# Kernel optimization log

Measured on AMD Instinct MI355X. Metric: run time of the kernel, lower is better.

## Reference

```python
import jax, jax.numpy as jnp
import numpy as np

N, E, ESM, H, OUT, L, NG = 20000, 640000, 1280, 128, 256, 3, 64
NV, EV = 4, 1  # node/edge vector channels
MSG_S, MSG_V = 2 * H + H, 2 * NV + EV   # 384, 9
UPD_S, UPD_V = 2 * H, 2 * NV            # 256, 8


def _safe_norm(v):
    # exact ||v|| with zero (not nan) gradient at v == 0
    n2 = jnp.sum(v * v, axis=-1)
    pos = n2 > 0
    return jnp.sqrt(jnp.where(pos, n2, 1.0)) * pos


def _normalize(x, eps=1e-12):
    n = _safe_norm(x)[..., None]
    return jnp.where(n > 0, x / jnp.maximum(n, eps), 0.0)


def _ln(x, g, b, eps=1e-5):
    m = x.mean(-1, keepdims=True)
    v = ((x - m) ** 2).mean(-1, keepdims=True)
    return (x - m) / jnp.sqrt(v + eps) * g + b


def _gvp(s, v, Wss, Wvs, Wsv, Wvv, g, b):
    # s: [M, Cs], v: [M, Cv, 3]
    vn = _safe_norm(v)                                        # [M, Cv]
    s_out = jax.nn.gelu(_ln(s @ Wss.T + vn @ Wvs.T, g, b), approximate=False)
    v_out = jnp.einsum('mic,oi->moc', v, Wvv)                 # [M, Cvo, 3]
    v_out = v_out * jax.nn.sigmoid(s @ Wsv.T)[:, :, None]     # gate from input s
    return s_out, v_out


def _compute_node_vectors(coords, cb):
    ca_cb = _normalize(cb - coords)
    ca_next = jnp.roll(coords, -1, axis=0)
    d = (ca_next - coords).at[-1].set(0.0)
    d = _normalize(d)
    normal = _normalize(jnp.cross(ca_cb, d))
    t = (ca_next - jnp.roll(coords, 1, axis=0)).at[0].set(0.0).at[-1].set(0.0)
    t = _normalize(t)
    return jnp.stack([ca_cb, d, normal, t], axis=1)           # [N, 4, 3]


def setup_inputs() -> dict:
    key = jax.random.key(0)
    ks = jax.random.split(key, 32)

    def w(k, shape):
        return (jax.random.normal(k, shape, jnp.float32) / np.sqrt(shape[-1])).astype(jnp.float32)

    inp = {
        'esm_features': jax.random.normal(ks[0], (N, ESM), jnp.float32),
        'geometric_features': jax.random.normal(ks[1], (N, 15), jnp.float32),
        'node_coords': jax.random.normal(ks[2], (N, 3), jnp.float32) * 10.0,
        'edge_index': jax.random.randint(ks[3], (2, E), 0, N, jnp.int32),
        'edge_attr': jax.random.normal(ks[4], (E, 16), jnp.float32),
        'batch_index': jnp.sort(jax.random.randint(ks[5], (N,), 0, NG, jnp.int32)),
        # projections
        'node_proj_W': w(ks[6], (H, ESM + 9)), 'node_proj_b': jnp.zeros((H,), jnp.float32),
        'edge_proj_W': w(ks[7], (H, 13)), 'edge_proj_b': jnp.zeros((H,), jnp.float32),
        # message GVP (stacked over L layers)
        'msg_Wss': w(ks[8], (L, H, MSG_S)), 'msg_Wvs': w(ks[9], (L, H, MSG_V)),
        'msg_Wsv': w(ks[10], (L, NV, MSG_S)), 'msg_Wvv': w(ks[11], (L, NV, MSG_V)),
        'msg_ln_g': jnp.ones((L, H), jnp.float32), 'msg_ln_b': jnp.zeros((L, H), jnp.float32),
        # update GVP
        'upd_Wss': w(ks[12], (L, H, UPD_S)), 'upd_Wvs': w(ks[13], (L, H, UPD_V)),
        'upd_Wsv': w(ks[14], (L, NV, UPD_S)), 'upd_Wvv': w(ks[15], (L, NV, UPD_V)),
        'upd_ln_g': jnp.ones((L, H), jnp.float32), 'upd_ln_b': jnp.zeros((L, H), jnp.float32),
        # heads
        'node_out_W': w(ks[16], (ESM, H)), 'node_out_b': jnp.zeros((ESM,), jnp.float32),
        'graph_out_W': w(ks[17], (OUT, H)), 'graph_out_b': jnp.zeros((OUT,), jnp.float32),
    }
    return inp


def reference(esm_features, geometric_features, node_coords, edge_index, edge_attr,
              batch_index, node_proj_W, node_proj_b, edge_proj_W, edge_proj_b,
              msg_Wss, msg_Wvs, msg_Wsv, msg_Wvv, msg_ln_g, msg_ln_b,
              upd_Wss, upd_Wvs, upd_Wsv, upd_Wvv, upd_ln_g, upd_ln_b,
              node_out_W, node_out_b, graph_out_W, graph_out_b):
    n = esm_features.shape[0]
    cb = geometric_features[:, 3:6]
    geo_scalar = geometric_features[:, 6:15]
    node_s = jnp.concatenate([esm_features, geo_scalar], -1) @ node_proj_W.T + node_proj_b
    node_v = _compute_node_vectors(node_coords, cb)
    edge_s = jnp.concatenate([edge_attr[:, 0:2], edge_attr[:, 5:]], -1) @ edge_proj_W.T + edge_proj_b
    edge_v = edge_attr[:, 2:5][:, None, :]                    # [E, 1, 3]
    src, dst = edge_index[0], edge_index[1]
    for l in range(msg_Wss.shape[0]):
        ms = jnp.concatenate([node_s[src], node_s[dst], edge_s], -1)   # [E, 3H]
        mv = jnp.concatenate([node_v[src], node_v[dst], edge_v], 1)    # [E, 9, 3]
        ms, mv = _gvp(ms, mv, msg_Wss[l], msg_Wvs[l], msg_Wsv[l], msg_Wvv[l],
                      msg_ln_g[l], msg_ln_b[l])
        ag_s = jnp.zeros((n, ms.shape[1]), ms.dtype).at[dst].add(ms)
        ag_v = jnp.zeros((n, mv.shape[1], 3), mv.dtype).at[dst].add(mv)
        us = jnp.concatenate([node_s, ag_s], -1)
        uv = jnp.concatenate([node_v, ag_v], 1)
        ns, nv = _gvp(us, uv, upd_Wss[l], upd_Wvs[l], upd_Wsv[l], upd_Wvv[l],
                      upd_ln_g[l], upd_ln_b[l])
        node_s = node_s + ns
        node_v = node_v + nv
    updated_nodes = node_s @ node_out_W.T + node_out_b
    gfeat = node_s @ graph_out_W.T + graph_out_b
    cnt = jax.ops.segment_sum(jnp.ones((n,), gfeat.dtype), batch_index, NG)
    graph_emb = jax.ops.segment_sum(gfeat, batch_index, NG) / jnp.maximum(cnt, 1.0)[:, None]
    return graph_emb, updated_nodes
```

## Files before the change

kernel.cpp:

```cpp
#include <hip/hip_runtime.h>
#include <math.h>

#define DEVI __device__ __forceinline__

namespace {

constexpr int NN = 20000;
constexpr int NE = 640000;

DEVI float gelu_f(float x){ return 0.5f*x*(1.0f+erff(x*0.70710678118654752440f)); }
DEVI float gelu_t(float x){
  float u = x*x;
  float z = x*(1.59576912f + 0.07135481f*u);
  return x / (1.f + __expf(-z));
}
DEVI float sigm(float x){ return 1.0f/(1.0f+expf(-x)); }
DEVI float sigm_f(float x){ return 1.0f/(1.0f+__expf(-x)); }
DEVI unsigned bf_rne(float f){ unsigned u=__float_as_uint(f); return (u + 0x7fffu + ((u>>16)&1u)) >> 16; }

struct F3{ float x,y,z; };
DEVI F3 sub3(F3 a, F3 b){ return F3{a.x-b.x, a.y-b.y, a.z-b.z}; }
DEVI F3 cross3(F3 a, F3 b){ return F3{a.y*b.z-a.z*b.y, a.z*b.x-a.x*b.z, a.x*b.y-a.y*b.x}; }
DEVI F3 snorm3(F3 v){
  float n2 = v.x*v.x+v.y*v.y+v.z*v.z;
  if(n2 > 0.f){ float inv = 1.0f/sqrtf(n2); return F3{v.x*inv, v.y*inv, v.z*inv}; }
  return F3{0.f,0.f,0.f};
}

__global__ void k_prep(const float* __restrict__ npW, const float* __restrict__ noW,
                       const float* __restrict__ goW,
                       const float* __restrict__ mWss, const float* __restrict__ mWvs,
                       const float* __restrict__ uWss, const float* __restrict__ uWvs,
                       float* __restrict__ Wt_np, float* __restrict__ Wt_no,
                       float* __restrict__ Wt_go,
                       float* __restrict__ Wt_mss, float* __restrict__ Wt_mvs,
                       float* __restrict__ Wt_uss, float* __restrict__ Wt_uvs){
  int b = blockIdx.x, t = threadIdx.x;
  const float* src; float* dst; int R,C,ld,base,elems;
  if(b<645){ src=npW; dst=Wt_np; R=128;C=1289;ld=1289; base=0; elems=164992; }
  else if(b<1285){ src=noW; dst=Wt_no; R=1280;C=128;ld=128; base=645; elems=163840; }
  else if(b<1413){ src=goW; dst=Wt_go; R=256;C=128;ld=128; base=1285; elems=32768; }
  else {
    int bb=b-1413; int l=bb/265; int r=bb-l*265;
    if(r<128){ src=mWss+(size_t)l*128*384; dst=Wt_mss+(size_t)l*256*128; R=128;C=256;ld=384; base=1413+l*265; elems=32768; }
    else if(r<133){ src=mWvs+(size_t)l*128*9; dst=Wt_mvs+(size_t)l*9*128; R=128;C=9;ld=9; base=1413+l*265+128; elems=1152; }
    else if(r<261){ src=uWss+(size_t)l*128*256; dst=Wt_uss+(size_t)l*256*128; R=128;C=256;ld=256; base=1413+l*265+133; elems=32768; }
    else { src=uWvs+(size_t)l*128*8; dst=Wt_uvs+(size_t)l*8*128; R=128;C=8;ld=8; base=1413+l*265+261; elems=1024; }
  }
  int idx=(b-base)*256+t;
  if(idx>=elems) return;
  int r=idx/C, c=idx%C;
  dst[c*R+r] = src[r*ld+c];
}

__global__ __launch_bounds__(256,4) void k_init(
                       const float* __restrict__ esm, const float* __restrict__ geo,
                       const float* __restrict__ Wt, const float* __restrict__ bias,
                       float* __restrict__ node_s){
  __shared__ float s_l[16][64];
  int t = threadIdx.x;
  int o = t&127, h = t>>7;
  int n0 = blockIdx.x*16;
  float acc[8];
#pragma unroll
  for(int i=0;i<8;i++) acc[i]=0.f;
  for(int k0=0;k0<1289;k0+=64){
    int kmax = (1289-k0 < 64) ? (1289-k0) : 64;
    for(int idx=t; idx<1024; idx+=256){
      int n = idx>>6, k = idx&63;
      float v = 0.f;
      int kk = k0+k;
      if(k < kmax){
        v = (kk<1280) ? esm[(size_t)(n0+n)*1280 + kk] : geo[(n0+n)*15 + 6 + (kk-1280)];
      }
      s_l[n][k] = v;
    }
    __syncthreads();
    int kq = kmax & ~3;
    for(int k=0;k<kq;k+=4){
      float w0 = Wt[(k0+k)*128+o];
      float w1 = Wt[(k0+k+1)*128+o];
      float w2 = Wt[(k0+k+2)*128+o];
      float w3 = Wt[(k0+k+3)*128+o];
#pragma unroll
      for(int n=0;n<8;n++){
        float4 s4 = *reinterpret_cast<const float4*>(&s_l[h*8+n][k]);
        acc[n] += s4.x*w0 + s4.y*w1 + s4.z*w2 + s4.w*w3;
      }
    }
    for(int k=kq;k<kmax;k++){
      float w = Wt[(k0+k)*128+o];
#pragma unroll
      for(int n=0;n<8;n++) acc[n] += s_l[h*8+n][k]*w;
    }
    __syncthreads();
  }
  float b = bias[o];
#pragma unroll
  for(int n=0;n<8;n++) node_s[(size_t)(n0+h*8+n)*128 + o] = acc[n] + b;
}

__global__ void k_nodevec(const float* __restrict__ coords, const float* __restrict__ geo,
                          float* __restrict__ node_v,
                          int* __restrict__ counts, int* __restrict__ cntg){
  int n = blockIdx.x*256 + threadIdx.x;
  if(n<64) cntg[n]=0;
  if(n>=NN) return;
  counts[n]=0;
  F3 c  {coords[n*3], coords[n*3+1], coords[n*3+2]};
  F3 cb {geo[n*15+3], geo[n*15+4], geo[n*15+5]};
  F3 cacb = snorm3(sub3(cb, c));
  F3 d{0.f,0.f,0.f};
  if(n < NN-1){
    F3 nx {coords[(n+1)*3], coords[(n+1)*3+1], coords[(n+1)*3+2]};
    d = snorm3(sub3(nx, c));
  }
  F3 nor = snorm3(cross3(cacb, d));
  F3 tv{0.f,0.f,0.f};
  if(n>0 && n<NN-1){
    F3 nx {coords[(n+1)*3], coords[(n+1)*3+1], coords[(n+1)*3+2]};
    F3 pv {coords[(n-1)*3], coords[(n-1)*3+1], coords[(n-1)*3+2]};
    tv = snorm3(sub3(nx, pv));
  }
  float* p = node_v + n*12;
  p[0]=cacb.x; p[1]=cacb.y; p[2]=cacb.z;
  p[3]=d.x;    p[4]=d.y;    p[5]=d.z;
  p[6]=nor.x;  p[7]=nor.y;  p[8]=nor.z;
  p[9]=tv.x;   p[10]=tv.y;  p[11]=tv.z;
}

__global__ void k_hist(const int* __restrict__ eidx, const int* __restrict__ batch,
                       int* __restrict__ counts, int* __restrict__ cntg){
  int i = blockIdx.x*256+threadIdx.x;
  if(i<NE) atomicAdd(&counts[eidx[NE+i]], 1);
  if(i<NN) atomicAdd(&cntg[batch[i]], 1);
}
__global__ void k_scan1(const int* __restrict__ counts, int* __restrict__ bsums){
  __shared__ int red[256];
  int b=blockIdx.x, t=threadIdx.x;
  int base=b*512;
  int v=0;
  for(int i=t;i<512;i+=256){ int g=base+i; if(g<NN) v+=counts[g]; }
  red[t]=v; __syncthreads();
  for(int s=128;s;s>>=1){ if(t<s) red[t]+=red[t+s]; __syncthreads(); }
  if(t==0) bsums[b]=red[0];
}
__global__ void k_scan23(const int* __restrict__ counts, const int* __restrict__ bsums,
                         int* __restrict__ offs, int* __restrict__ cursor){
  __shared__ int c_l[512];
  int b=blockIdx.x, t=threadIdx.x, base=b*512;
  for(int i=t;i<512;i+=256){ int g=base+i; c_l[i] = (g<NN)? counts[g]:0; }
  __syncthreads();
  if(t==0){
    int run=0;
    for(int i=0;i<b;i++) run += bsums[i];
    for(int i=0;i<512;i++){
      int g=base+i;
      if(g<NN){ offs[g]=run; cursor[g]=run; }
      run += c_l[i];
    }
    if(b==39) offs[NN]=run;
  }
}
__global__ void k_fill(const int* __restrict__ eidx, int* __restrict__ cursor,
                       const float* __restrict__ eattr,
                       int* __restrict__ srcp, float* __restrict__ ea_s){
  int e = blockIdx.x*256+threadIdx.x;
  if(e>=NE) return;
  int d = eidx[NE+e];
  int s = eidx[e];
  int pos = atomicAdd(&cursor[d], 1);
  srcp[pos] = s;
  const float4* src4 = reinterpret_cast<const float4*>(eattr + (size_t)e*16);
  float4* dst4 = reinterpret_cast<float4*>(ea_s + (size_t)pos*16);
  dst4[0]=src4[0]; dst4[1]=src4[1]; dst4[2]=src4[2]; dst4[3]=src4[3];
}

__global__ __launch_bounds__(256,4) void k_pre(
                      const float* __restrict__ node_s, const float* __restrict__ node_v,
                      const float* __restrict__ Wt_ss, const float* __restrict__ Wt_vs,
                      const float* __restrict__ Wsv, const float* __restrict__ Wvv,
                      float* __restrict__ P_a, float* __restrict__ P_b,
                      float* __restrict__ G_a, float* __restrict__ G_b,
                      float* __restrict__ V_a, float* __restrict__ V_b){
  __shared__ float s_l[16][128];
  __shared__ float nv_l[16][4];
  __shared__ float uv[16][12];
  int t = threadIdx.x;
  int n0 = blockIdx.x*16;
  for(int idx=t; idx<2048; idx+=256){
    int n = idx>>7, k = idx&127;
    s_l[n][k] = node_s[(size_t)(n0+n)*128 + k];
  }
  if(t<192){ int n=t/12, k=t%12; uv[n][k] = node_v[(n0+n)*12+k]; }
  __syncthreads();
  if(t<64){
    int n=t>>2, j=t&3;
    float x=uv[n][j*3], y=uv[n][j*3+1], z=uv[n][j*3+2];
    float n2=x*x+y*y+z*z;
    nv_l[n][j] = n2>0.f ? sqrtf(n2) : 0.f;
  }
  if(t<192){
    int n=t/12, k=t%12, c=k/3, x=k-c*3;
    float va=0.f, vb=0.f;
#pragma unroll
    for(int j=0;j<4;j++){
      float vv = uv[n][j*3+x];
      va += Wvv[c*9+j]*vv;
      vb += Wvv[c*9+4+j]*vv;
    }
    V_a[(n0+n)*12+k]=va; V_b[(n0+n)*12+k]=vb;
  }
  if(t<128){
    int n=t>>3, c=(t>>1)&3, hh=t&1;
    const float* w = Wsv + c*384 + hh*128;
    float g=0.f;
    for(int k=0;k<128;k+=4){
      float4 s4 = *reinterpret_cast<const float4*>(&s_l[n][k]);
      g = fmaf(s4.x,w[k],g); g = fmaf(s4.y,w[k+1],g);
      g = fmaf(s4.z,w[k+2],g); g = fmaf(s4.w,w[k+3],g);
    }
    (hh ? G_b : G_a)[(n0+n)*4+c] = g;
  }
  __syncthreads();
  int o = t&127, h = t>>7;
  float acc[16];
#pragma unroll
  for(int i=0;i<16;i++) acc[i]=0.f;
  const float* Wb = Wt_ss + h*128*128;
  for(int k=0;k<128;k+=4){
    float w0=Wb[(k+0)*128+o], w1=Wb[(k+1)*128+o], w2=Wb[(k+2)*128+o], w3=Wb[(k+3)*128+o];
#pragma unroll
    for(int n=0;n<16;n++){
      float4 s4 = *reinterpret_cast<const float4*>(&s_l[n][k]);
      acc[n] = fmaf(s4.x,w0,acc[n]); acc[n] = fmaf(s4.y,w1,acc[n]);
      acc[n] = fmaf(s4.z,w2,acc[n]); acc[n] = fmaf(s4.w,w3,acc[n]);
    }
  }
  const float* Wv = Wt_vs + h*4*128;
#pragma unroll
  for(int j=0;j<4;j++){
    float w = Wv[j*128+o];
#pragma unroll
    for(int n=0;n<16;n++) acc[n] += nv_l[n][j]*w;
  }
  float* P = h ? P_b : P_a;
#pragma unroll
  for(int n=0;n<16;n++) P[(size_t)(n0+n)*128+o] = acc[n];
}

__global__ void k_econst3(const float* __restrict__ mWss, const float* __restrict__ mWvs,
                          const float* __restrict__ mWsv, const float* __restrict__ mWvv,
                          const float* __restrict__ Wep, const float* __restrict__ epb,
                          float* __restrict__ econ){
  int l = blockIdx.x;
  const float* Wss = mWss + (size_t)l*128*384;
  const float* Wvs = mWvs + (size_t)l*128*9;
  const float* Wsv = mWsv + (size_t)l*4*384;
  const float* Wvv = mWvv + (size_t)l*4*9;
  float* ec = econ + (size_t)l*2048;
  int t=threadIdx.x;
  for(int idx=t; idx<13*128; idx+=256){
    int j=idx>>7, o=idx&127;
    float s=0.f;
    for(int k=0;k<128;k++) s += Wss[o*384+256+k]*Wep[k*13+j];
    ec[j*128+o]=s;
  }
  for(int o=t;o<128;o+=256){
    float s=0.f;
    for(int k=0;k<128;k++) s += Wss[o*384+256+k]*epb[k];
    ec[1664+o]=s;
    ec[1792+o]=Wvs[o*9+8];
  }
  if(t<52){ int c=t/13,j=t%13; float s=0.f; for(int k=0;k<128;k++) s+=Wsv[c*384+256+k]*Wep[k*13+j]; ec[1920+t]=s; }
  if(t<4){ float s=0.f; for(int k=0;k<128;k++) s+=Wsv[t*384+256+k]*epb[k]; ec[1972+t]=s; ec[1976+t]=Wvv[t*9+8]; }
}

__global__ __launch_bounds__(256,4) void k_edge(
    const float* __restrict__ ea_s, const float* __restrict__ ec,
    unsigned* __restrict__ preS2, float* __restrict__ preG){
  int t = threadIdx.x;
  int lane = t&63;
  int wid = blockIdx.x*4 + (t>>6);
  float mex[13], mey[13];
#pragma unroll
  for(int j=0;j<13;j++){ mex[j]=ec[j*128+lane]; mey[j]=ec[j*128+64+lane]; }
  float bx=ec[1664+lane], by=ec[1664+64+lane];
  float w8x=ec[1792+lane], w8y=ec[1792+64+lane];
  int cg = (lane<4)?lane:0;
  float grc[13];
#pragma unroll
  for(int j=0;j<13;j++) grc[j]=ec[1920+cg*13+j];
  float gb = ec[1972+cg];
  int e00 = wid*8;
#pragma unroll 2
  for(int i=0;i<8;i++){
    int e = e00+i;
    const float4* ea = reinterpret_cast<const float4*>(ea_s + (size_t)e*16);
    float4 A0=ea[0], A1=ea[1], A2=ea[2], A3=ea[3];
    float e0=A0.x,e1=A0.y,e2=A1.y,e3=A1.z,e4=A1.w,
          e5=A2.x,e6=A2.y,e7=A2.z,e8=A2.w,e9=A3.x,
          e10=A3.y,e11=A3.z,e12=A3.w;
    float evx=A0.z, evy=A0.w, evz=A1.x;
    float en2 = evx*evx+evy*evy+evz*evz;
    float evn = en2>0.f ? sqrtf(en2) : 0.f;
    float px = fmaf(evn,w8x,bx);
    float py = fmaf(evn,w8y,by);
    px=fmaf(mex[0],e0,px);   py=fmaf(mey[0],e0,py);
    px=fmaf(mex[1],e1,px);   py=fmaf(mey[1],e1,py);
    px=fmaf(mex[2],e2,px);   py=fmaf(mey[2],e2,py);
    px=fmaf(mex[3],e3,px);   py=fmaf(mey[3],e3,py);
    px=fmaf(mex[4],e4,px);   py=fmaf(mey[4],e4,py);
    px=fmaf(mex[5],e5,px);   py=fmaf(mey[5],e5,py);
    px=fmaf(mex[6],e6,px);   py=fmaf(mey[6],e6,py);
    px=fmaf(mex[7],e7,px);   py=fmaf(mey[7],e7,py);
    px=fmaf(mex[8],e8,px);   py=fmaf(mey[8],e8,py);
    px=fmaf(mex[9],e9,px);   py=fmaf(mey[9],e9,py);
    px=fmaf(mex[10],e10,px); py=fmaf(mey[10],e10,py);
    px=fmaf(mex[11],e11,px); py=fmaf(mey[11],e11,py);
    px=fmaf(mex[12],e12,px); py=fmaf(mey[12],e12,py);
    preS2[(size_t)e*64+lane] = bf_rne(px) | (bf_rne(py)<<16);
    if(lane<4){
      float g=gb;
      g=fmaf(grc[0],e0,g);  g=fmaf(grc[1],e1,g);  g=fmaf(grc[2],e2,g);
      g=fmaf(grc[3],e3,g);  g=fmaf(grc[4],e4,g);  g=fmaf(grc[5],e5,g);
      g=fmaf(grc[6],e6,g);  g=fmaf(grc[7],e7,g);  g=fmaf(grc[8],e8,g);
      g=fmaf(grc[9],e9,g);  g=fmaf(grc[10],e10,g); g=fmaf(grc[11],e11,g);
      g=fmaf(grc[12],e12,g);
      preG[(size_t)e*8+lane] = g;
    } else if(lane<7){
      float evv = (lane==4)?evx:((lane==5)?evy:evz);
      preG[(size_t)e*8+lane] = evv;
    }
  }
}

#define DECLST(P) unsigned P##w=0; float P##pax=0.f,P##pay=0.f,P##g8=0.f,P##ev=0.f,P##ga=0.f,P##va=0.f;
#define LOADST(P, IDX) do{ int _p=(IDX); int _s=srcp[_p]; \
  P##w   = preS2[(size_t)_p*64 + lane]; \
  P##pax = P_a[(size_t)_s*128+lane]; P##pay = P_a[(size_t)_s*128+64+lane]; \
  if(lane<12){ P##g8 = preG[(size_t)_p*8+cv]; P##ev = preG[(size_t)_p*8+4+xv]; \
               P##ga = G_a[(size_t)_s*4+cv];  P##va = V_a[(size_t)_s*12+lane]; } \
}while(0)
#define COMPUTE(P) do{ \
  float px = __uint_as_float(P##w<<16); \
  float py = __uint_as_float(P##w & 0xffff0000u); \
  float pre0 = px + P##pax + PBx; \
  float pre1 = py + P##pay + PBy; \
  float sm = pre0+pre1; \
  float sq = pre0*pre0 + pre1*pre1; \
  _Pragma("unroll") \
  for(int m=32;m;m>>=1){ sm += __shfl_xor(sm,m); sq += __shfl_xor(sq,m); } \
  float mean = sm*0.0078125f; \
  float var  = fmaf(sq,0.0078125f, -mean*mean); \
  float rstd = rsqrtf((var>0.f?var:0.f) + 1e-5f); \
  accx += gelu_t(fmaf((pre0-mean)*rstd, LGx, LBx)); \
  accy += gelu_t(fmaf((pre1-mean)*rstd, LGy, LBy)); \
  if(lane<12){ \
    float g = P##g8 + P##ga + gbn; \
    float gt = sigm_f(g); \
    avk = fmaf(fmaf(wvc, P##ev, P##va + vbk), gt, avk); \
  } \
}while(0)

__global__ __launch_bounds__(256,4) void k_msg(
                      const float* __restrict__ P_a, const float* __restrict__ P_b,
                      const float* __restrict__ G_a, const float* __restrict__ G_b,
                      const float* __restrict__ V_a, const float* __restrict__ V_b,
                      const unsigned* __restrict__ preS2, const float* __restrict__ preG,
                      const int* __restrict__ srcp, const int* __restrict__ offs,
                      const float* __restrict__ ec,
                      const float* __restrict__ lng, const float* __restrict__ lnb,
                      float* __restrict__ ag_s, float* __restrict__ ag_v){
  int t = threadIdx.x;
  int n = blockIdx.x*4 + (t>>6);
  int lane = t&63;
  float PBx = P_b[(size_t)n*128+lane], PBy = P_b[(size_t)n*128+64+lane];
  float LGx = lng[lane], LGy = lng[64+lane];
  float LBx = lnb[lane], LBy = lnb[64+lane];
  int cv = lane/3, xv = lane - cv*3;
  float vbk=0.f, gbn=0.f, wvc=0.f;
  if(lane<12){
    vbk = V_b[(size_t)n*12+lane];
    gbn = G_b[(size_t)n*4+cv];
    wvc = ec[1976+cv];
  }
  float accx=0.f, accy=0.f, avk=0.f;
  int beg = offs[n], end = offs[n+1];
  DECLST(a_) DECLST(b_)
  int idx = beg;
  if(beg < end) LOADST(a_, beg);
  while(idx + 1 < end){
    LOADST(b_, idx+1);
    COMPUTE(a_);
    if(idx + 2 < end) LOADST(a_, idx+2);
    COMPUTE(b_);
    idx += 2;
  }
  if(idx < end) COMPUTE(a_);
  ag_s[(size_t)n*128+lane]    = accx;
  ag_s[(size_t)n*128+64+lane] = accy;
  if(lane<12) ag_v[(size_t)n*12+lane] = avk;
}

__global__ __launch_bounds__(256,4) void k_update(
                         float* __restrict__ node_s, float* __restrict__ node_v,
                         const float* __restrict__ ag_s, const float* __restrict__ ag_v,
                         const float* __restrict__ Wt_ss, const float* __restrict__ Wt_vs,
                         const float* __restrict__ Wsv, const float* __restrict__ Wvv,
                         const float* __restrict__ lng, const float* __restrict__ lnb){
  __shared__ float us[16][260];
  __shared__ float pre[16][129];
  __shared__ float uv[16][24];
  __shared__ float uvn[16][8];
  __shared__ float stats[16][2];
  __shared__ float gate_l[16][4];
  int t = threadIdx.x;
  int n0 = blockIdx.x*16;
  for(int idx=t; idx<2048; idx+=256){
    int n = idx>>7, k = idx&127;
    us[n][k]     = node_s[(size_t)(n0+n)*128+k];
    us[n][128+k] = ag_s[(size_t)(n0+n)*128+k];
  }
  for(int idx=t; idx<384; idx+=256){
    int n = idx/24, k = idx%24;
    uv[n][k] = (k<12) ? node_v[(n0+n)*12+k] : ag_v[(n0+n)*12 + (k-12)];
  }
  __syncthreads();
  if(t<128){
    int n=t>>3, j=t&7;
    float x=uv[n][j*3], y=uv[n][j*3+1], z=uv[n][j*3+2];
    float n2=x*x+y*y+z*z;
    uvn[n][j] = n2>0.f ? sqrtf(n2) : 0.f;
  }
  __syncthreads();
  int o = t&127, h = t>>7;
  float acc[8];
#pragma unroll
  for(int i=0;i<8;i++) acc[i]=0.f;
  for(int k=0;k<256;k+=4){
    float w0=Wt_ss[(k+0)*128+o], w1=Wt_ss[(k+1)*128+o], w2=Wt_ss[(k+2)*128+o], w3=Wt_ss[(k+3)*128+o];
#pragma unroll
    for(int i=0;i<8;i++){
      float4 s4 = *reinterpret_cast<const float4*>(&us[h*8+i][k]);
      acc[i] = fmaf(s4.x,w0,acc[i]); acc[i] = fmaf(s4.y,w1,acc[i]);
      acc[i] = fmaf(s4.z,w2,acc[i]); acc[i] = fmaf(s4.w,w3,acc[i]);
    }
  }
#pragma unroll
  for(int j=0;j<8;j++){
    float w = Wt_vs[j*128+o];
#pragma unroll
    for(int i=0;i<8;i++) acc[i] += uvn[h*8+i][j]*w;
  }
#pragma unroll
  for(int i=0;i<8;i++) pre[h*8+i][o] = acc[i];
  __syncthreads();
  {
    int n = t>>4, p = t&15;
    float s=0.f;
#pragma unroll
    for(int q=0;q<8;q++) s += pre[n][p*8+q];
#pragma unroll
    for(int m=8;m;m>>=1) s += __shfl_xor(s,m);
    float mean = s*(1.f/128.f);
    float v=0.f;
#pragma unroll
    for(int q=0;q<8;q++){ float d=pre[n][p*8+q]-mean; v += d*d; }
#pragma unroll
    for(int m=8;m;m>>=1) v += __shfl_xor(v,m);
    if(p==0){ stats[n][0]=mean; stats[n][1]=rsqrtf(v*(1.f/128.f)+1e-5f); }
  }
  __syncthreads();
  {
    float LG = lng[o], LB = lnb[o];
#pragma unroll
    for(int i=0;i<8;i++){
      int n = h*8+i;
      float hh = (pre[n][o]-stats[n][0])*stats[n][1]*LG + LB;
      node_s[(size_t)(n0+n)*128+o] += gelu_f(hh);
    }
  }
  {
    int n = t>>4, c = t&3, p = (t>>2)&3;
    float g=0.f;
    int kb = p*64;
    for(int k=0;k<64;k+=4){
      float4 s4 = *reinterpret_cast<const float4*>(&us[n][kb+k]);
      g = fmaf(s4.x,Wsv[c*256+kb+k],g);   g = fmaf(s4.y,Wsv[c*256+kb+k+1],g);
      g = fmaf(s4.z,Wsv[c*256+kb+k+2],g); g = fmaf(s4.w,Wsv[c*256+kb+k+3],g);
    }
    g += __shfl_xor(g,4);
    g += __shfl_xor(g,8);
    if(p==0) gate_l[n][c] = sigm(g);
  }
  __syncthreads();
  if(t<192){
    int n = t/12, k = t%12, c = k/3, x = k-c*3;
    float s=0.f;
#pragma unroll
    for(int j=0;j<8;j++) s += Wvv[c*8+j]*uv[n][j*3+x];
    node_v[(n0+n)*12+k] += s*gate_l[n][c];
  }
}

__global__ __launch_bounds__(256,4) void k_outg(
                      const float* __restrict__ node_s, const float* __restrict__ Wt_no,
                      const float* __restrict__ nob, const float* __restrict__ Wt_go,
                      const int* __restrict__ batch, float* __restrict__ gacc,
                      float* __restrict__ out){
  __shared__ float s_l[16][128];
  __shared__ int b_l[16];
  int t = threadIdx.x;
  int n0 = blockIdx.x*16;
  int y = blockIdx.y;
  for(int idx=t; idx<2048; idx+=256){
    int n=idx>>7, k=idx&127;
    s_l[n][k] = node_s[(size_t)(n0+n)*128+k];
  }
  if(y==5 && t<16) b_l[t]=batch[n0+t];
  __syncthreads();
  if(y<5){
    int o = y*256 + t;
    float acc[16];
#pragma unroll
    for(int i=0;i<16;i++) acc[i]=0.f;
    for(int k=0;k<128;k+=4){
      float w0=Wt_no[(k+0)*1280+o], w1=Wt_no[(k+1)*1280+o], w2=Wt_no[(k+2)*1280+o], w3=Wt_no[(k+3)*1280+o];
#pragma unroll
      for(int n=0;n<16;n++){
        float4 s4 = *reinterpret_cast<const float4*>(&s_l[n][k]);
        acc[n] = fmaf(s4.x,w0,acc[n]); acc[n] = fmaf(s4.y,w1,acc[n]);
        acc[n] = fmaf(s4.z,w2,acc[n]); acc[n] = fmaf(s4.w,w3,acc[n]);
      }
    }
    float b = nob[o];
#pragma unroll
    for(int n=0;n<16;n++) out[16384 + (size_t)(n0+n)*1280 + o] = acc[n]+b;
  } else {
    int o=t;
    float acc[16];
#pragma unroll
    for(int i=0;i<16;i++) acc[i]=0.f;
    for(int k=0;k<128;k+=4){
      float w0=Wt_go[(k+0)*256+o], w1=Wt_go[(k+1)*256+o], w2=Wt_go[(k+2)*256+o], w3=Wt_go[(k+3)*256+o];
#pragma unroll
      for(int n=0;n<16;n++){
        float4 s4 = *reinterpret_cast<const float4*>(&s_l[n][k]);
        acc[n] = fmaf(s4.x,w0,acc[n]); acc[n] = fmaf(s4.y,w1,acc[n]);
        acc[n] = fmaf(s4.z,w2,acc[n]); acc[n] = fmaf(s4.w,w3,acc[n]);
      }
    }
    float run=0.f; int cur=b_l[0];
#pragma unroll
    for(int n=0;n<16;n++){
      int g=b_l[n];
      if(g!=cur){ atomicAdd(&gacc[cur*256+o], run); run=0.f; cur=g; }
      run += acc[n];
    }
    atomicAdd(&gacc[cur*256+o], run);
  }
}

__global__ void k_gfin(const float* __restrict__ gacc, const int* __restrict__ cntg,
                       const float* __restrict__ gob, float* __restrict__ out){
  int g=blockIdx.x, o=threadIdx.x;
  int c=cntg[g];
  out[g*256+o] = (c>0) ? (gacc[g*256+o]/(float)c + gob[o]) : 0.f;
}

}

extern "C" void kernel_launch(void* const* d_in, const int* in_sizes, int n_in,
                              void* d_out, int out_size, void* d_ws, size_t ws_size,
                              hipStream_t stream){
  (void)in_sizes; (void)n_in; (void)out_size;
  const float* esm   = (const float*)d_in[0];
  const float* geo   = (const float*)d_in[1];
  const float* coords= (const float*)d_in[2];
  const int*   eidx  = (const int*)d_in[3];
  const float* eattr = (const float*)d_in[4];
  const int*   batch = (const int*)d_in[5];
  const float* npW   = (const float*)d_in[6];
  const float* npb   = (const float*)d_in[7];
  const float* epW   = (const float*)d_in[8];
  const float* epb   = (const float*)d_in[9];
  const float* mWss  = (const float*)d_in[10];
  const float* mWvs  = (const float*)d_in[11];
  const float* mWsv  = (const float*)d_in[12];
  const float* mWvv  = (const float*)d_in[13];
  const float* mlg   = (const float*)d_in[14];
  const float* mlb   = (const float*)d_in[15];
  const float* uWss  = (const float*)d_in[16];
  const float* uWvs  = (const float*)d_in[17];
  const float* uWsv  = (const float*)d_in[18];
  const float* uWvv  = (const float*)d_in[19];
  const float* ulg   = (const float*)d_in[20];
  const float* ulb   = (const float*)d_in[21];
  const float* noW   = (const float*)d_in[22];
  const float* nob   = (const float*)d_in[23];
  const float* goW   = (const float*)d_in[24];
  const float* gob   = (const float*)d_in[25];
  float* out = (float*)d_out;

  char* base = (char*)d_ws;
  size_t off = 0;
  auto ALLOC = [&](size_t bytes)->char*{
    char* p = base + off;
    off = (off + bytes + 255) & ~(size_t)255;
    return p;
  };
  float* node_s = (float*)ALLOC((size_t)NN*128*4);
  float* P_a    = (float*)ALLOC((size_t)NN*128*4);
  float* P_b    = (float*)ALLOC((size_t)NN*128*4);
  float* ag_s   = (float*)ALLOC((size_t)NN*128*4);
  float* node_v = (float*)ALLOC((size_t)NN*12*4);
  float* ag_v   = (float*)ALLOC((size_t)NN*12*4);
  float* V_a    = (float*)ALLOC((size_t)NN*12*4);
  float* V_b    = (float*)ALLOC((size_t)NN*12*4);
  float* G_a    = (float*)ALLOC((size_t)NN*4*4);
  float* G_b    = (float*)ALLOC((size_t)NN*4*4);
  float* Wt_np  = (float*)ALLOC((size_t)1289*128*4);
  float* Wt_no  = (float*)ALLOC((size_t)128*1280*4);
  float* Wt_go  = (float*)ALLOC((size_t)128*256*4);
  float* Wt_mss = (float*)ALLOC((size_t)3*256*128*4);
  float* Wt_mvs = (float*)ALLOC((size_t)3*9*128*4);
  float* Wt_uss = (float*)ALLOC((size_t)3*256*128*4);
  float* Wt_uvs = (float*)ALLOC((size_t)3*8*128*4);
  float* econ   = (float*)ALLOC((size_t)3*2048*4);
  float* gacc   = (float*)ALLOC((size_t)64*256*4);
  int* counts = (int*)ALLOC((size_t)NN*4);
  int* offs   = (int*)ALLOC((size_t)(NN+1)*4);
  int* cursor = (int*)ALLOC((size_t)NN*4);
  int* bsums  = (int*)ALLOC((size_t)64*4);
  int* cntg   = (int*)ALLOC((size_t)64*4);
  int* srcp   = (int*)ALLOC((size_t)NE*4);
  float* ea_s = (float*)ALLOC((size_t)NE*16*4);
  unsigned* preS2 = (unsigned*)ALLOC((size_t)NE*64*4);
  float* preG     = (float*)ALLOC((size_t)NE*8*4);
  if(off > ws_size) return;

  hipMemsetAsync(gacc, 0, (size_t)64*256*4, stream);

  k_prep<<<2208,256,0,stream>>>(npW, noW, goW, mWss, mWvs, uWss, uWvs,
                                Wt_np, Wt_no, Wt_go, Wt_mss, Wt_mvs, Wt_uss, Wt_uvs);
  k_init<<<1250,256,0,stream>>>(esm, geo, Wt_np, npb, node_s);
  k_nodevec<<<79,256,0,stream>>>(coords, geo, node_v, counts, cntg);
  k_hist<<<2500,256,0,stream>>>(eidx, batch, counts, cntg);
  k_scan1<<<40,256,0,stream>>>(counts, bsums);
  k_scan23<<<40,256,0,stream>>>(counts, bsums, offs, cursor);
  k_fill<<<2500,256,0,stream>>>(eidx, cursor, eattr, srcp, ea_s);
  k_econst3<<<3,256,0,stream>>>(mWss, mWvs, mWsv, mWvv, epW, epb, econ);

  for(int l=0;l<3;l++){
    k_pre<<<1250,256,0,stream>>>(node_s, node_v,
                                 Wt_mss + (size_t)l*256*128, Wt_mvs + (size_t)l*9*128,
                                 mWsv + (size_t)l*4*384, mWvv + (size_t)l*4*9,
                                 P_a, P_b, G_a, G_b, V_a, V_b);
    k_edge<<<20000,256,0,stream>>>(ea_s, econ + (size_t)l*2048, preS2, preG);
    k_msg<<<5000,256,0,stream>>>(P_a, P_b, G_a, G_b, V_a, V_b, preS2, preG, srcp, offs,
                                 econ + (size_t)l*2048, mlg + (size_t)l*128, mlb + (size_t)l*128,
                                 ag_s, ag_v);
    k_update<<<1250,256,0,stream>>>(node_s, node_v, ag_s, ag_v,
                                    Wt_uss + (size_t)l*256*128, Wt_uvs + (size_t)l*8*128,
                                    uWsv + (size_t)l*4*256, uWvv + (size_t)l*4*8,
                                    ulg + (size_t)l*128, ulb + (size_t)l*128);
  }
  k_outg<<<dim3(1250,6),256,0,stream>>>(node_s, Wt_no, nob, Wt_go, batch, gacc, out);
  k_gfin<<<64,256,0,stream>>>(gacc, cntg, gob, out);
}
```

Before: 1.716 ms.

## Use bf16 MFMA for the input node projection GEMM

Rewrites the 20000x1289 by 1289x128 input projection to stage bf16 tiles of activations and weights in LDS and compute them with 16x16x32 bf16 MFMA instructions, with 64 nodes per block. The weight prep now converts the projection weights to bf16 in place instead of transposing them. This moves the scalar fp32 FMA loop onto matrix cores, at the cost of bf16 rounding of the ESM features and weights, which reduces precision of the initial node embeddings. The grid drops from 1250 to 313 blocks, which is only a little more than the number of CUs and may leave the device underfilled.

```diff
diff --git a/kernel.cpp b/kernel.cpp
--- a/kernel.cpp
+++ b/kernel.cpp
@@ -7,6 +7,9 @@
 
 constexpr int NN = 20000;
 constexpr int NE = 640000;
+
+typedef __attribute__((ext_vector_type(8))) short s8v;
+typedef __attribute__((ext_vector_type(4))) float f4v;
 
 DEVI float gelu_f(float x){ return 0.5f*x*(1.0f+erff(x*0.70710678118654752440f)); }
 DEVI float gelu_t(float x){
@@ -31,21 +34,25 @@
                        const float* __restrict__ goW,
                        const float* __restrict__ mWss, const float* __restrict__ mWvs,
                        const float* __restrict__ uWss, const float* __restrict__ uWvs,
-                       float* __restrict__ Wt_np, float* __restrict__ Wt_no,
+                       unsigned short* __restrict__ npW_bf, float* __restrict__ Wt_no,
                        float* __restrict__ Wt_go,
                        float* __restrict__ Wt_mss, float* __restrict__ Wt_mvs,
                        float* __restrict__ Wt_uss, float* __restrict__ Wt_uvs){
   int b = blockIdx.x, t = threadIdx.x;
+  if(b >= 1563){
+    int idx = (b-1563)*256 + t;
+    if(idx < 128*1289) npW_bf[idx] = (unsigned short)bf_rne(npW[idx]);
+    return;
+  }
   const float* src; float* dst; int R,C,ld,base,elems;
-  if(b<645){ src=npW; dst=Wt_np; R=128;C=1289;ld=1289; base=0; elems=164992; }
-  else if(b<1285){ src=noW; dst=Wt_no; R=1280;C=128;ld=128; base=645; elems=163840; }
-  else if(b<1413){ src=goW; dst=Wt_go; R=256;C=128;ld=128; base=1285; elems=32768; }
+  if(b<640){ src=noW; dst=Wt_no; R=1280;C=128;ld=128; base=0; elems=163840; }
+  else if(b<768){ src=goW; dst=Wt_go; R=256;C=128;ld=128; base=640; elems=32768; }
   else {
-    int bb=b-1413; int l=bb/265; int r=bb-l*265;
-    if(r<128){ src=mWss+(size_t)l*128*384; dst=Wt_mss+(size_t)l*256*128; R=128;C=256;ld=384; base=1413+l*265; elems=32768; }
-    else if(r<133){ src=mWvs+(size_t)l*128*9; dst=Wt_mvs+(size_t)l*9*128; R=128;C=9;ld=9; base=1413+l*265+128; elems=1152; }
-    else if(r<261){ src=uWss+(size_t)l*128*256; dst=Wt_uss+(size_t)l*256*128; R=128;C=256;ld=256; base=1413+l*265+133; elems=32768; }
-    else { src=uWvs+(size_t)l*128*8; dst=Wt_uvs+(size_t)l*8*128; R=128;C=8;ld=8; base=1413+l*265+261; elems=1024; }
+    int bb=b-768; int l=bb/265; int r=bb-l*265;
+    if(r<128){ src=mWss+(size_t)l*128*384; dst=Wt_mss+(size_t)l*256*128; R=128;C=256;ld=384; base=768+l*265; elems=32768; }
+    else if(r<133){ src=mWvs+(size_t)l*128*9; dst=Wt_mvs+(size_t)l*9*128; R=128;C=9;ld=9; base=768+l*265+128; elems=1152; }
+    else if(r<261){ src=uWss+(size_t)l*128*256; dst=Wt_uss+(size_t)l*256*128; R=128;C=256;ld=256; base=768+l*265+133; elems=32768; }
+    else { src=uWvs+(size_t)l*128*8; dst=Wt_uvs+(size_t)l*8*128; R=128;C=8;ld=8; base=768+l*265+261; elems=1024; }
   }
   int idx=(b-base)*256+t;
   if(idx>=elems) return;
@@ -53,51 +60,69 @@
   dst[c*R+r] = src[r*ld+c];
 }
 
-__global__ __launch_bounds__(256,4) void k_init(
-                       const float* __restrict__ esm, const float* __restrict__ geo,
-                       const float* __restrict__ Wt, const float* __restrict__ bias,
-                       float* __restrict__ node_s){
-  __shared__ float s_l[16][64];
+__global__ __launch_bounds__(256,2) void k_init(
+    const float* __restrict__ esm, const float* __restrict__ geo,
+    const unsigned short* __restrict__ npW_bf, const float* __restrict__ bias,
+    float* __restrict__ node_s){
+  __shared__ unsigned short A_lds[64][136];
+  __shared__ unsigned short B_lds[128][136];
   int t = threadIdx.x;
-  int o = t&127, h = t>>7;
-  int n0 = blockIdx.x*16;
-  float acc[8];
-#pragma unroll
-  for(int i=0;i<8;i++) acc[i]=0.f;
-  for(int k0=0;k0<1289;k0+=64){
-    int kmax = (1289-k0 < 64) ? (1289-k0) : 64;
-    for(int idx=t; idx<1024; idx+=256){
-      int n = idx>>6, k = idx&63;
-      float v = 0.f;
-      int kk = k0+k;
-      if(k < kmax){
-        v = (kk<1280) ? esm[(size_t)(n0+n)*1280 + kk] : geo[(n0+n)*15 + 6 + (kk-1280)];
+  int n0 = blockIdx.x*64;
+  int wv = t>>6, lane = t&63;
+  int kpair = t&63;
+  int rb = t>>6;
+  f4v acc[8];
+#pragma unroll
+  for(int i=0;i<8;i++) acc[i] = (f4v){0.f,0.f,0.f,0.f};
+  for(int k0=0; k0<1408; k0+=128){
+#pragma unroll
+    for(int i=0;i<16;i++){
+      int r = rb + 4*i;
+      int row = n0 + r;
+      int kk = k0 + 2*kpair;
+      float v0=0.f, v1=0.f;
+      if(row < NN){
+        if(kk < 1280)        v0 = esm[(size_t)row*1280+kk];
+        else if(kk < 1289)   v0 = geo[row*15+6+(kk-1280)];
+        if(kk+1 < 1280)      v1 = esm[(size_t)row*1280+kk+1];
+        else if(kk+1 < 1289) v1 = geo[row*15+6+(kk+1-1280)];
       }
-      s_l[n][k] = v;
+      *reinterpret_cast<unsigned*>(&A_lds[r][2*kpair]) = bf_rne(v0) | (bf_rne(v1)<<16);
+    }
+#pragma unroll
+    for(int i=0;i<32;i++){
+      int o = rb + 4*i;
+      int kk = k0 + 2*kpair;
+      unsigned w0 = (kk<1289)   ? (unsigned)npW_bf[(size_t)o*1289+kk]   : 0u;
+      unsigned w1 = (kk+1<1289) ? (unsigned)npW_bf[(size_t)o*1289+kk+1] : 0u;
+      *reinterpret_cast<unsigned*>(&B_lds[o][2*kpair]) = w0 | (w1<<16);
     }
     __syncthreads();
-    int kq = kmax & ~3;
-    for(int k=0;k<kq;k+=4){
-      float w0 = Wt[(k0+k)*128+o];
-      float w1 = Wt[(k0+k+1)*128+o];
-      float w2 = Wt[(k0+k+2)*128+o];
-      float w3 = Wt[(k0+k+3)*128+o];
-#pragma unroll
-      for(int n=0;n<8;n++){
-        float4 s4 = *reinterpret_cast<const float4*>(&s_l[h*8+n][k]);
-        acc[n] += s4.x*w0 + s4.y*w1 + s4.z*w2 + s4.w*w3;
+    int arow = wv*16 + (lane&15);
+    int kb = (lane>>4)*8;
+#pragma unroll
+    for(int s=0;s<4;s++){
+      s8v a = *reinterpret_cast<const s8v*>(&A_lds[arow][s*32+kb]);
+#pragma unroll
+      for(int nt=0;nt<8;nt++){
+        s8v b = *reinterpret_cast<const s8v*>(&B_lds[nt*16+(lane&15)][s*32+kb]);
+        acc[nt] = __builtin_amdgcn_mfma_f32_16x16x32_bf16(a, b, acc[nt], 0,0,0);
       }
     }
-    for(int k=kq;k<kmax;k++){
-      float w = Wt[(k0+k)*128+o];
-#pragma unroll
-      for(int n=0;n<8;n++) acc[n] += s_l[h*8+n][k]*w;
-    }
     __syncthreads();
   }
-  float b = bias[o];
-#pragma unroll
-  for(int n=0;n<8;n++) node_s[(size_t)(n0+h*8+n)*128 + o] = acc[n] + b;
+  int col = lane&15;
+  int r4 = (lane>>4)*4;
+#pragma unroll
+  for(int nt=0;nt<8;nt++){
+    int o = nt*16+col;
+    float bsv = bias[o];
+#pragma unroll
+    for(int r=0;r<4;r++){
+      int row = n0 + wv*16 + r4 + r;
+      if(row<NN) node_s[(size_t)row*128+o] = acc[nt][r] + bsv;
+    }
+  }
 }
 
 __global__ void k_nodevec(const float* __restrict__ coords, const float* __restrict__ geo,
@@ -620,7 +645,7 @@
   float* V_b    = (float*)ALLOC((size_t)NN*12*4);
   float* G_a    = (float*)ALLOC((size_t)NN*4*4);
   float* G_b    = (float*)ALLOC((size_t)NN*4*4);
-  float* Wt_np  = (float*)ALLOC((size_t)1289*128*4);
+  unsigned short* npW_bf = (unsigned short*)ALLOC((size_t)128*1289*2);
   float* Wt_no  = (float*)ALLOC((size_t)128*1280*4);
   float* Wt_go  = (float*)ALLOC((size_t)128*256*4);
   float* Wt_mss = (float*)ALLOC((size_t)3*256*128*4);
@@ -643,8 +668,8 @@
   hipMemsetAsync(gacc, 0, (size_t)64*256*4, stream);
 
   k_prep<<<2208,256,0,stream>>>(npW, noW, goW, mWss, mWvs, uWss, uWvs,
-                                Wt_np, Wt_no, Wt_go, Wt_mss, Wt_mvs, Wt_uss, Wt_uvs);
-  k_init<<<1250,256,0,stream>>>(esm, geo, Wt_np, npb, node_s);
+                                npW_bf, Wt_no, Wt_go, Wt_mss, Wt_mvs, Wt_uss, Wt_uvs);
+  k_init<<<313,256,0,stream>>>(esm, geo, npW_bf, npb, node_s);
   k_nodevec<<<79,256,0,stream>>>(coords, geo, node_v, counts, cntg);
   k_hist<<<2500,256,0,stream>>>(eidx, batch, counts, cntg);
   k_scan1<<<40,256,0,stream>>>(counts, bsums);
```

After: 1.705 ms. Within noise of the previous version (-0.7%).
